# Optimization experiments

Measured on AMD Instinct MI355X. Metric: run time of the kernel, lower is better.

Reference implementation:

```python
import jax, jax.numpy as jnp
import numpy as np

D_MODEL, D_K, D_V, N_HEADS = 1024, 64, 64, 16
B, T = 4, 2048


def _xavier(key, shape, gain):
    fan_in, fan_out = shape[0], shape[1]
    a = gain * np.sqrt(6.0 / (fan_in + fan_out))
    return jax.random.uniform(key, shape, jnp.float32, -a, a)


def setup_inputs() -> dict:
    key = jax.random.key(0)
    ks = jax.random.split(key, 6)
    H, dk, dv, d = N_HEADS, D_K, D_V, D_MODEL
    # weights stored as (in, out) so y = x @ W matches torch nn.Linear math
    return {
        "x": jax.random.normal(ks[0], (B, T, d), jnp.float32),
        "W_q": _xavier(ks[1], (d, H * dk), 0.1),
        "W_k": _xavier(ks[2], (d, H * dk), 0.1),
        "W_v": _xavier(ks[3], (d, H * dv), 0.1),
        "W_gate": _xavier(ks[4], (d, H * dk), 0.01),
        "b_gate": jnp.full((H * dk,), 3.0, jnp.float32),
        "W_o": _xavier(ks[5], (H * dv, d), 0.1),
    }


def reference(x, W_q, W_k, W_v, W_gate, b_gate, W_o):
    Bn, Tn, d = x.shape
    H, dk, dv = N_HEADS, D_K, D_V
    q = (x @ W_q).reshape(Bn, Tn, H, dk)
    k = (x @ W_k).reshape(Bn, Tn, H, dk)
    v = (x @ W_v).reshape(Bn, Tn, H, dv)
    a = jax.nn.sigmoid(x @ W_gate + b_gate).reshape(Bn, Tn, H, dk)

    # scan over time: carry S is (B, H, dk, dv)
    def step(S, qkva):
        q_t, k_t, v_t, a_t = qkva  # each (B, H, d*)
        S = a_t[..., None] * S + k_t[..., None] * v_t[..., None, :]
        o_t = jnp.einsum('bhk,bhkv->bhv', q_t, S)
        return S, o_t

    S0 = jnp.zeros((Bn, H, dk, dv), x.dtype)
    # move time axis to front for scan
    qs = jnp.moveaxis(q, 1, 0)
    ks_ = jnp.moveaxis(k, 1, 0)
    vs = jnp.moveaxis(v, 1, 0)
    as_ = jnp.moveaxis(a, 1, 0)
    _, outs = jax.lax.scan(step, S0, (qs, ks_, vs, as_))  # (T, B, H, dv)
    out = jnp.moveaxis(outs, 0, 1).reshape(Bn, Tn, H * dv)
    return out @ W_o
```

## Files before the change

### kernel.cpp

```cpp
#include <hip/hip_runtime.h>
#include <hip/hip_bf16.h>

#define DM   1024
#define NH   16
#define TSEQ 2048
#define BBATCH 4
#define MM   (BBATCH*TSEQ)

typedef unsigned short USH;
typedef __attribute__((ext_vector_type(8))) short bf16x8;
typedef __attribute__((ext_vector_type(4))) float f32x4;

__device__ __forceinline__ USH f2bf(float f) {
  __hip_bfloat16 h = __float2bfloat16(f);
  return __builtin_bit_cast(USH, h);
}
__device__ __forceinline__ float bflo(unsigned u) { return __uint_as_float(u << 16); }
__device__ __forceinline__ float bfhi(unsigned u) { return __uint_as_float(u & 0xffff0000u); }

__device__ __forceinline__ void load16_lds(const void* g, void* l) {
  __builtin_amdgcn_global_load_lds(
      (const __attribute__((address_space(1))) unsigned int*)g,
      (__attribute__((address_space(3))) unsigned int*)l, 16, 0, 0);
}

__global__ void cvt_x(const float* __restrict__ x, USH* __restrict__ xb) {
  int i = (blockIdx.x * blockDim.x + threadIdx.x) * 4;
  float4 f = *(const float4*)(x + i);
  ushort4 u;
  u.x = f2bf(f.x); u.y = f2bf(f.y); u.z = f2bf(f.z); u.w = f2bf(f.w);
  *(ushort4*)(xb + i) = u;
}

__global__ void trans_cvt(const float* __restrict__ w0, const float* __restrict__ w1,
                          const float* __restrict__ w2, const float* __restrict__ w3,
                          const float* __restrict__ w4,
                          USH* __restrict__ wcatT, USH* __restrict__ woT) {
  int z = blockIdx.z;
  const float* src = (z == 0) ? w0 : (z == 1) ? w1 : (z == 2) ? w2 : (z == 3) ? w3 : w4;
  USH* dst = (z < 4) ? (wcatT + (size_t)z * 1024 * 1024) : woT;
  __shared__ float tile[32][33];
  int x = blockIdx.x * 32 + threadIdx.x;
  int y = blockIdx.y * 32;
  for (int j = threadIdx.y; j < 32; j += 8)
    tile[j][threadIdx.x] = src[(size_t)(y + j) * 1024 + x];
  __syncthreads();
  int x2 = blockIdx.y * 32 + threadIdx.x;
  int y2 = blockIdx.x * 32;
  for (int j = threadIdx.y; j < 32; j += 8)
    dst[(size_t)(y2 + j) * 1024 + x2] = f2bf(tile[threadIdx.x][j]);
}

template <int EPI>
__global__ __launch_bounds__(256, 2) void gemm_bt(
    const USH* __restrict__ A, const USH* __restrict__ B, int K,
    USH* __restrict__ q_out, USH* __restrict__ k_out, USH* __restrict__ v_out,
    USH* __restrict__ a_out, const float* __restrict__ bias,
    float* __restrict__ c_out) {
  __shared__ short As[128 * 64];
  __shared__ short Bs[128 * 64];
  const int tid = threadIdx.x;
  const int wave = tid >> 6;
  const int lane = tid & 63;
  const int bm = blockIdx.y, bn = blockIdx.x;
  const int wm = (wave >> 1) * 64;
  const int wn = (wave & 1) * 64;

  f32x4 acc[4][4];
#pragma unroll
  for (int i = 0; i < 4; i++)
#pragma unroll
    for (int j = 0; j < 4; j++) acc[i][j] = (f32x4){0.f, 0.f, 0.f, 0.f};

  const int srow = wave * 8 + (lane >> 3);
  const int scol = (lane & 7) * 8;

  for (int k0 = 0; k0 < K; k0 += 64) {
#pragma unroll
    for (int i = 0; i < 4; ++i) {
      int row = i * 32 + srow;
      const USH* ga = A + (size_t)(bm * 128 + row) * K + k0 + scol;
      const USH* gb = B + (size_t)(bn * 128 + row) * K + k0 + scol;
      int lofs = __builtin_amdgcn_readfirstlane((i * 32 + wave * 8) * 64);
      load16_lds(ga, (void*)(As + lofs));
      load16_lds(gb, (void*)(Bs + lofs));
    }
    __syncthreads();
#pragma unroll
    for (int ks = 0; ks < 64; ks += 32) {
      bf16x8 af[4], bf[4];
#pragma unroll
      for (int i = 0; i < 4; i++)
        af[i] = *(const bf16x8*)&As[(wm + i * 16 + (lane & 15)) * 64 + ks + (lane >> 4) * 8];
#pragma unroll
      for (int j = 0; j < 4; j++)
        bf[j] = *(const bf16x8*)&Bs[(wn + j * 16 + (lane & 15)) * 64 + ks + (lane >> 4) * 8];
#pragma unroll
      for (int i = 0; i < 4; i++)
#pragma unroll
        for (int j = 0; j < 4; j++)
          acc[i][j] = __builtin_amdgcn_mfma_f32_16x16x32_bf16(af[i], bf[j], acc[i][j], 0, 0, 0);
    }
    __syncthreads();
  }

  const int r0 = (lane >> 4) * 4;
  const int cc = lane & 15;
#pragma unroll
  for (int i = 0; i < 4; i++) {
#pragma unroll
    for (int j = 0; j < 4; j++) {
      int gn = bn * 128 + wn + j * 16 + cc;
#pragma unroll
      for (int r = 0; r < 4; r++) {
        int gm = bm * 128 + wm + i * 16 + r0 + r;
        float val = acc[i][j][r];
        if (EPI == 0) {
          c_out[(size_t)gm * 1024 + gn] = val;
        } else {
          int which = gn >> 10, cn = gn & 1023;
          size_t idx = (size_t)gm * 1024 + cn;
          if (which == 0)      q_out[idx] = f2bf(val);
          else if (which == 1) k_out[idx] = f2bf(val);
          else if (which == 2) v_out[idx] = f2bf(val);
          else {
            float s = 1.0f / (1.0f + __expf(-(val + bias[cn])));
            a_out[idx] = (USH)(s * 65535.0f + 0.5f);
          }
        }
      }
    }
  }
}

__global__ __launch_bounds__(256, 3) void gla_chunk(
    USH* __restrict__ qb, const USH* __restrict__ kb, const USH* __restrict__ vb,
    const USH* __restrict__ au, USH* __restrict__ ob,
    float* __restrict__ SB, float* __restrict__ Dc) {
  const int bh = blockIdx.x >> 5, ch = blockIdx.x & 31;
  const size_t base = (size_t)(bh >> 4) * TSEQ * 1024 + (size_t)(bh & 15) * 64;
  const int row0 = ch * 64;
  const int tid = threadIdx.x, wv = tid >> 6, ln = tid & 63;

  __shared__ __align__(16) char smem[54528];
  USH* Qs  = (USH*)smem;
  USH* Ks  = (USH*)(smem + 9216);
  USH* Kht = (USH*)(smem + 18432);
  USH* Vt  = (USH*)(smem + 27648);
  float* psum = (float*)(smem + 27648);
  USH* Ps  = (USH*)(smem + 36864);
  USH* so  = (USH*)(smem + 46080);
  float* Ag = (float*)(smem + 36864);

  {
    const int c1 = tid & 63, sg = tid >> 6;
    float lp[16], p = 1.f;
#pragma unroll
    for (int r = 0; r < 16; ++r) {
      float a = (float)au[base + (size_t)(row0 + sg * 16 + r) * 1024 + c1] * (1.f / 65535.f);
      p *= a;
      lp[r] = p;
    }
    psum[sg * 64 + c1] = p;
    __syncthreads();
    float pre = 1.f;
    for (int s2 = 0; s2 < sg; ++s2) pre *= psum[s2 * 64 + c1];
#pragma unroll
    for (int r = 0; r < 16; ++r) Ag[(sg * 16 + r) * 65 + c1] = pre * lp[r];
  }
  __syncthreads();
  if (tid < 64) Dc[((size_t)bh * 32 + ch) * 64 + tid] = Ag[63 * 65 + tid];

  {
    const int rr = tid >> 4, cg = (tid & 15) * 4;
    float AC[4];
#pragma unroll
    for (int i = 0; i < 4; i++) AC[i] = Ag[63 * 65 + cg + i];
#pragma unroll
    for (int j = 0; j < 4; ++j) {
      int row = rr + j * 16;
      size_t g = base + (size_t)(row0 + row) * 1024 + cg;
      uint2 qv = *(const uint2*)(qb + g);
      uint2 kv = *(const uint2*)(kb + g);
      uint2 vv = *(const uint2*)(vb + g);
      float A0 = Ag[row * 65 + cg], A1 = Ag[row * 65 + cg + 1];
      float A2 = Ag[row * 65 + cg + 2], A3 = Ag[row * 65 + cg + 3];
      ushort4 qt;
      qt.x = f2bf(bflo(qv.x) * A0); qt.y = f2bf(bfhi(qv.x) * A1);
      qt.z = f2bf(bflo(qv.y) * A2); qt.w = f2bf(bfhi(qv.y) * A3);
      *(ushort4*)&Qs[row * 72 + cg] = qt;
      *(ushort4*)(qb + g) = qt;
      float R0 = 1.f / A0, R1 = 1.f / A1, R2 = 1.f / A2, R3 = 1.f / A3;
      float kt0 = bflo(kv.x) * R0, kt1 = bfhi(kv.x) * R1;
      float kt2 = bflo(kv.y) * R2, kt3 = bfhi(kv.y) * R3;
      ushort4 kt;
      kt.x = f2bf(kt0); kt.y = f2bf(kt1); kt.z = f2bf(kt2); kt.w = f2bf(kt3);
      *(ushort4*)&Ks[row * 72 + cg] = kt;
      Kht[(cg + 0) * 72 + row] = f2bf(kt0 * AC[0]);
      Kht[(cg + 1) * 72 + row] = f2bf(kt1 * AC[1]);
      Kht[(cg + 2) * 72 + row] = f2bf(kt2 * AC[2]);
      Kht[(cg + 3) * 72 + row] = f2bf(kt3 * AC[3]);
      Vt[(cg + 0) * 72 + row] = (USH)(vv.x & 0xffff);
      Vt[(cg + 1) * 72 + row] = (USH)(vv.x >> 16);
      Vt[(cg + 2) * 72 + row] = (USH)(vv.y & 0xffff);
      Vt[(cg + 3) * 72 + row] = (USH)(vv.y >> 16);
    }
  }
  __syncthreads();

  const int q4 = (ln >> 4) * 4, cc = ln & 15, m16 = ln & 15;

  f32x4 pc[4];
#pragma unroll
  for (int n = 0; n < 4; n++) pc[n] = (f32x4){0.f, 0.f, 0.f, 0.f};
#pragma unroll
  for (int ks = 0; ks < 64; ks += 32) {
    bf16x8 aq = *(const bf16x8*)&Qs[(wv * 16 + m16) * 72 + ks + (ln >> 4) * 8];
#pragma unroll
    for (int n = 0; n < 4; ++n) {
      bf16x8 bk = *(const bf16x8*)&Ks[(n * 16 + m16) * 72 + ks + (ln >> 4) * 8];
      pc[n] = __builtin_amdgcn_mfma_f32_16x16x32_bf16(aq, bk, pc[n], 0, 0, 0);
    }
  }
#pragma unroll
  for (int n = 0; n < 4; ++n) {
    int s = n * 16 + cc;
#pragma unroll
    for (int r = 0; r < 4; ++r) {
      int t = wv * 16 + q4 + r;
      Ps[t * 72 + s] = f2bf(s <= t ? pc[n][r] : 0.f);
    }
  }

  f32x4 sc[4];
#pragma unroll
  for (int n = 0; n < 4; n++) sc[n] = (f32x4){0.f, 0.f, 0.f, 0.f};
#pragma unroll
  for (int ks = 0; ks < 64; ks += 32) {
    bf16x8 ak = *(const bf16x8*)&Kht[(wv * 16 + m16) * 72 + ks + (ln >> 4) * 8];
#pragma unroll
    for (int n = 0; n < 4; ++n) {
      bf16x8 bv = *(const bf16x8*)&Vt[(n * 16 + m16) * 72 + ks + (ln >> 4) * 8];
      sc[n] = __builtin_amdgcn_mfma_f32_16x16x32_bf16(ak, bv, sc[n], 0, 0, 0);
    }
  }
  {
    float* sbp = SB + ((size_t)bh * 32 + ch) * 4096;
#pragma unroll
    for (int n = 0; n < 4; ++n)
#pragma unroll
      for (int r = 0; r < 4; ++r)
        sbp[(wv * 16 + q4 + r) * 64 + n * 16 + cc] = sc[n][r];
  }
  __syncthreads();

  f32x4 oc[4];
#pragma unroll
  for (int n = 0; n < 4; n++) oc[n] = (f32x4){0.f, 0.f, 0.f, 0.f};
#pragma unroll
  for (int ks = 0; ks < 64; ks += 32) {
    bf16x8 ap = *(const bf16x8*)&Ps[(wv * 16 + m16) * 72 + ks + (ln >> 4) * 8];
#pragma unroll
    for (int n = 0; n < 4; ++n) {
      bf16x8 bv = *(const bf16x8*)&Vt[(n * 16 + m16) * 72 + ks + (ln >> 4) * 8];
      oc[n] = __builtin_amdgcn_mfma_f32_16x16x32_bf16(ap, bv, oc[n], 0, 0, 0);
    }
  }
#pragma unroll
  for (int n = 0; n < 4; ++n)
#pragma unroll
    for (int r = 0; r < 4; ++r)
      so[(wv * 16 + q4 + r) * 66 + n * 16 + cc] = f2bf(oc[n][r]);
  __syncthreads();
#pragma unroll
  for (int j = 0; j < 4; ++j) {
    int row = (tid >> 4) + j * 16, cg = (tid & 15) * 4;
    unsigned a = *(const unsigned*)&so[row * 66 + cg];
    unsigned b = *(const unsigned*)&so[row * 66 + cg + 2];
    size_t g = base + (size_t)(row0 + row) * 1024 + cg;
    *(unsigned*)(ob + g) = a;
    *(unsigned*)(ob + g + 2) = b;
  }
}

__global__ __launch_bounds__(256, 2) void gla_stitch_c(float* __restrict__ SB,
                                                       const float* __restrict__ Dc) {
  const int bh = blockIdx.x >> 2, kq = blockIdx.x & 3;
  const int tid = threadIdx.x;
  const int kk = kq * 16 + (tid >> 4);
  const int v4 = (tid & 15) * 4;
  float4 s = {0.f, 0.f, 0.f, 0.f};
  const size_t sOff = ((size_t)bh * 32) * 4096 + (size_t)kk * 64 + v4;
  const size_t dOff = ((size_t)bh * 32) * 64 + kk;
  float4 l = *(float4*)(SB + sOff);
  float D = Dc[dOff];
  for (int chn = 0; chn < 32; ++chn) {
    float4 ln2 = {0.f, 0.f, 0.f, 0.f};
    float Dn = 0.f;
    if (chn + 1 < 32) {
      ln2 = *(float4*)(SB + sOff + (size_t)(chn + 1) * 4096);
      Dn = Dc[dOff + (size_t)(chn + 1) * 64];
    }
    *(float4*)(SB + sOff + (size_t)chn * 4096) = s;
    s.x = fmaf(D, s.x, l.x); s.y = fmaf(D, s.y, l.y);
    s.z = fmaf(D, s.z, l.z); s.w = fmaf(D, s.w, l.w);
    l = ln2; D = Dn;
  }
}

__global__ __launch_bounds__(256, 4) void gla_corr(
    const USH* __restrict__ qtb, const float* __restrict__ SB, USH* __restrict__ ob) {
  const int bh = blockIdx.y, chn = blockIdx.x + 1;
  const size_t base = (size_t)(bh >> 4) * TSEQ * 1024 + (size_t)(bh & 15) * 64;
  const int trow0 = chn * 64;
  const int tid = threadIdx.x;
  __shared__ float ss[64 * 64];
  __shared__ USH qs[64][72];
  const float* sp = SB + ((size_t)bh * 32 + chn) * 4096;
  for (int i = tid; i < 1024; i += 256)
    *((float4*)ss + i) = *((const float4*)sp + i);
#pragma unroll
  for (int j = 0; j < 4; ++j) {
    int i = tid + 256 * j;
    int row = i >> 4, cg = (i & 15) * 4;
    *(uint2*)&qs[row][cg] = *(const uint2*)(qtb + base + (size_t)(trow0 + row) * 1024 + cg);
  }
  __syncthreads();
  const int row = tid >> 2, vg = (tid & 3) * 16;
  float acc[16];
#pragma unroll
  for (int i = 0; i < 16; i++) acc[i] = 0.f;
  for (int k0 = 0; k0 < 64; k0 += 8) {
    uint4 qv = *(const uint4*)&qs[row][k0];
    float qf[8];
    qf[0] = bflo(qv.x); qf[1] = bfhi(qv.x);
    qf[2] = bflo(qv.y); qf[3] = bfhi(qv.y);
    qf[4] = bflo(qv.z); qf[5] = bfhi(qv.z);
    qf[6] = bflo(qv.w); qf[7] = bfhi(qv.w);
#pragma unroll
    for (int j = 0; j < 8; ++j) {
      const float* sr = &ss[(k0 + j) * 64 + vg];
      float4 s0 = *(const float4*)(sr + 0), s1 = *(const float4*)(sr + 4);
      float4 s2 = *(const float4*)(sr + 8), s3 = *(const float4*)(sr + 12);
      acc[0] = fmaf(qf[j], s0.x, acc[0]);   acc[1] = fmaf(qf[j], s0.y, acc[1]);
      acc[2] = fmaf(qf[j], s0.z, acc[2]);   acc[3] = fmaf(qf[j], s0.w, acc[3]);
      acc[4] = fmaf(qf[j], s1.x, acc[4]);   acc[5] = fmaf(qf[j], s1.y, acc[5]);
      acc[6] = fmaf(qf[j], s1.z, acc[6]);   acc[7] = fmaf(qf[j], s1.w, acc[7]);
      acc[8] = fmaf(qf[j], s2.x, acc[8]);   acc[9] = fmaf(qf[j], s2.y, acc[9]);
      acc[10] = fmaf(qf[j], s2.z, acc[10]); acc[11] = fmaf(qf[j], s2.w, acc[11]);
      acc[12] = fmaf(qf[j], s3.x, acc[12]); acc[13] = fmaf(qf[j], s3.y, acc[13]);
      acc[14] = fmaf(qf[j], s3.z, acc[14]); acc[15] = fmaf(qf[j], s3.w, acc[15]);
    }
  }
  USH* op = ob + base + (size_t)(trow0 + row) * 1024 + vg;
#pragma unroll
  for (int g = 0; g < 4; ++g) {
    ushort4 o4 = *(ushort4*)(op + g * 4);
    o4.x = f2bf(bflo((unsigned)o4.x) + acc[g * 4 + 0]);
    o4.y = f2bf(bflo((unsigned)o4.y) + acc[g * 4 + 1]);
    o4.z = f2bf(bflo((unsigned)o4.z) + acc[g * 4 + 2]);
    o4.w = f2bf(bflo((unsigned)o4.w) + acc[g * 4 + 3]);
    *(ushort4*)(op + g * 4) = o4;
  }
}

extern "C" void kernel_launch(void* const* d_in, const int* in_sizes, int n_in,
                              void* d_out, int out_size, void* d_ws, size_t ws_size,
                              hipStream_t stream) {
  const float* x  = (const float*)d_in[0];
  const float* Wq = (const float*)d_in[1];
  const float* Wk = (const float*)d_in[2];
  const float* Wv = (const float*)d_in[3];
  const float* Wg = (const float*)d_in[4];
  const float* bg = (const float*)d_in[5];
  const float* Wo = (const float*)d_in[6];
  float* out = (float*)d_out;

  char* ws = (char*)d_ws;
  size_t off = 0;
  auto alloc = [&](size_t bytes) {
    char* p = ws + off;
    off += (bytes + 255) & ~(size_t)255;
    return p;
  };
  USH* xb   = (USH*)alloc((size_t)MM * DM * 2);
  USH* WoT  = (USH*)alloc((size_t)1024 * 1024 * 2);
  USH* qb   = (USH*)alloc((size_t)MM * DM * 2);
  USH* kb   = (USH*)alloc((size_t)MM * DM * 2);
  USH* vb   = (USH*)alloc((size_t)MM * DM * 2);
  USH* au   = (USH*)alloc((size_t)MM * DM * 2);
  float* Dc = (float*)alloc((size_t)64 * 32 * 64 * 4);
  float* SB = (float*)alloc((size_t)64 * 32 * 4096 * 4);
  USH* WcatT = (USH*)SB;
  USH* ob = xb;

  cvt_x<<<(MM * DM) / 1024, 256, 0, stream>>>(x, xb);
  trans_cvt<<<dim3(32, 32, 5), dim3(32, 8), 0, stream>>>(Wq, Wk, Wv, Wg, Wo, WcatT, WoT);
  gemm_bt<1><<<dim3(32, 64), 256, 0, stream>>>(xb, WcatT, 1024, qb, kb, vb, au, bg, nullptr);
  gla_chunk<<<2048, 256, 0, stream>>>(qb, kb, vb, au, ob, SB, Dc);
  gla_stitch_c<<<256, 256, 0, stream>>>(SB, Dc);
  gla_corr<<<dim3(31, 64), 256, 0, stream>>>(qb, SB, ob);
  gemm_bt<0><<<dim3(8, 64), 256, 0, stream>>>(ob, WoT, 1024, nullptr, nullptr, nullptr,
                                              nullptr, nullptr, out);
}
```

Measured before the change: 295.4 us.

## Swizzle GEMM LDS tiles and stage epilogue through LDS for vectorized stores

Applies an XOR swizzle to the K-column chunk index when staging A and B tiles into LDS and when reading MFMA fragments, to reduce LDS bank conflicts. The epilogue now writes results into a padded LDS buffer and then emits coalesced 16-byte global stores, instead of scattered 2- or 4-byte stores. The gate bias is loaded once per column and the destination buffer is chosen per block rather than per element. This adds extra barriers and LDS traffic in the epilogue, and the fp32 path stages two halves in sequence.

Measured after the change: 271.8 us. 8.0% less time.

```diff
diff --git a/kernel.cpp b/kernel.cpp
--- a/kernel.cpp
+++ b/kernel.cpp
@@ -57,8 +57,9 @@
     USH* __restrict__ q_out, USH* __restrict__ k_out, USH* __restrict__ v_out,
     USH* __restrict__ a_out, const float* __restrict__ bias,
     float* __restrict__ c_out) {
-  __shared__ short As[128 * 64];
-  __shared__ short Bs[128 * 64];
+  __shared__ __align__(16) char smem[34816];
+  short* As = (short*)smem;
+  short* Bs = (short*)(smem + 16384);
   const int tid = threadIdx.x;
   const int wave = tid >> 6;
   const int lane = tid & 63;
@@ -73,7 +74,7 @@
     for (int j = 0; j < 4; j++) acc[i][j] = (f32x4){0.f, 0.f, 0.f, 0.f};
 
   const int srow = wave * 8 + (lane >> 3);
-  const int scol = (lane & 7) * 8;
+  const int scol = ((lane & 7) ^ (lane >> 3)) * 8;
 
   for (int k0 = 0; k0 < K; k0 += 64) {
 #pragma unroll
@@ -86,15 +87,18 @@
       load16_lds(gb, (void*)(Bs + lofs));
     }
     __syncthreads();
+    const int m16 = lane & 15;
+    const int sw = lane & 7;
+    const int kc = lane >> 4;
 #pragma unroll
     for (int ks = 0; ks < 64; ks += 32) {
       bf16x8 af[4], bf[4];
 #pragma unroll
       for (int i = 0; i < 4; i++)
-        af[i] = *(const bf16x8*)&As[(wm + i * 16 + (lane & 15)) * 64 + ks + (lane >> 4) * 8];
+        af[i] = *(const bf16x8*)&As[(wm + i * 16 + m16) * 64 + ((((ks >> 3) + kc) ^ sw) << 3)];
 #pragma unroll
       for (int j = 0; j < 4; j++)
-        bf[j] = *(const bf16x8*)&Bs[(wn + j * 16 + (lane & 15)) * 64 + ks + (lane >> 4) * 8];
+        bf[j] = *(const bf16x8*)&Bs[(wn + j * 16 + m16) * 64 + ((((ks >> 3) + kc) ^ sw) << 3)];
 #pragma unroll
       for (int i = 0; i < 4; i++)
 #pragma unroll
@@ -106,29 +110,61 @@
 
   const int r0 = (lane >> 4) * 4;
   const int cc = lane & 15;
-#pragma unroll
-  for (int i = 0; i < 4; i++) {
-#pragma unroll
-    for (int j = 0; j < 4; j++) {
-      int gn = bn * 128 + wn + j * 16 + cc;
-#pragma unroll
-      for (int r = 0; r < 4; r++) {
-        int gm = bm * 128 + wm + i * 16 + r0 + r;
-        float val = acc[i][j][r];
-        if (EPI == 0) {
-          c_out[(size_t)gm * 1024 + gn] = val;
-        } else {
-          int which = gn >> 10, cn = gn & 1023;
-          size_t idx = (size_t)gm * 1024 + cn;
-          if (which == 0)      q_out[idx] = f2bf(val);
-          else if (which == 1) k_out[idx] = f2bf(val);
-          else if (which == 2) v_out[idx] = f2bf(val);
-          else {
-            float s = 1.0f / (1.0f + __expf(-(val + bias[cn])));
-            a_out[idx] = (USH)(s * 65535.0f + 0.5f);
+  if (EPI == 1) {
+    USH* ep = (USH*)smem;
+    const int which = bn >> 3;
+    float bj[4];
+    if (which == 3) {
+#pragma unroll
+      for (int j = 0; j < 4; j++) bj[j] = bias[(bn & 7) * 128 + wn + j * 16 + cc];
+    }
+#pragma unroll
+    for (int i = 0; i < 4; i++)
+#pragma unroll
+      for (int j = 0; j < 4; j++)
+#pragma unroll
+        for (int r = 0; r < 4; r++) {
+          float val = acc[i][j][r];
+          USH o;
+          if (which == 3) {
+            float s = 1.0f / (1.0f + __expf(-(val + bj[j])));
+            o = (USH)(s * 65535.0f + 0.5f);
+          } else {
+            o = f2bf(val);
           }
+          ep[(wm + i * 16 + r0 + r) * 136 + wn + j * 16 + cc] = o;
         }
+    __syncthreads();
+    USH* dst = (which == 0) ? q_out : (which == 1) ? k_out : (which == 2) ? v_out : a_out;
+    const int rr = tid >> 4, ccol = (tid & 15) * 8;
+#pragma unroll
+    for (int it = 0; it < 8; ++it) {
+      int row = it * 16 + rr;
+      uint4 vd = *(const uint4*)&ep[row * 136 + ccol];
+      *(uint4*)(dst + (size_t)(bm * 128 + row) * 1024 + (bn & 7) * 128 + ccol) = vd;
+    }
+  } else {
+    float* epf = (float*)smem;
+#pragma unroll
+    for (int h = 0; h < 2; ++h) {
+      if (wm == h * 64) {
+#pragma unroll
+        for (int i = 0; i < 4; i++)
+#pragma unroll
+          for (int j = 0; j < 4; j++)
+#pragma unroll
+            for (int r = 0; r < 4; r++)
+              epf[(i * 16 + r0 + r) * 132 + wn + j * 16 + cc] = acc[i][j][r];
       }
+      __syncthreads();
+      const int rr = tid >> 5, c4 = (tid & 31) * 4;
+#pragma unroll
+      for (int it = 0; it < 8; ++it) {
+        int row = it * 8 + rr;
+        float4 vd = *(const float4*)&epf[row * 132 + c4];
+        *(float4*)(c_out + (size_t)(bm * 128 + h * 64 + row) * 1024 + bn * 128 + c4) = vd;
+      }
+      if (h == 0) __syncthreads();
     }
   }
 }
```
